# Optimization experiments

Measured on AMD Instinct MI355X. Metric: run time of the kernel, lower is better.

The kernel has to match this reference:

```python
import jax, jax.numpy as jnp
import numpy as np

NQ = 4
NL = 3
# Z-expectation sign table: state axis order = wire order, reshape(-1) => wire 0 is MSB
_bits = (np.arange(2 ** NQ)[:, None] >> np.arange(NQ - 1, -1, -1)) & 1
Z_SIGNS = jnp.asarray((1 - 2 * _bits).astype(np.float32))  # (16, 4)
_CNOT = jnp.asarray(np.array([[1, 0, 0, 0], [0, 1, 0, 0], [0, 0, 0, 1], [0, 0, 1, 0]],
                             dtype=np.complex64).reshape(2, 2, 2, 2))


def _rx(t):
    c = jnp.cos(t / 2).astype(jnp.complex64)
    s = (-1j) * jnp.sin(t / 2).astype(jnp.complex64)
    return jnp.stack([jnp.stack([c, s]), jnp.stack([s, c])])


def _rot(phi, theta, omega):
    # PennyLane Rot = RZ(omega) @ RY(theta) @ RZ(phi)
    ez = jnp.exp(-0.5j * phi.astype(jnp.complex64))
    zero = jnp.zeros_like(ez)
    rz1 = jnp.stack([jnp.stack([ez, zero]), jnp.stack([zero, jnp.conj(ez)])])
    c = jnp.cos(theta / 2).astype(jnp.complex64)
    s = jnp.sin(theta / 2).astype(jnp.complex64)
    ry = jnp.stack([jnp.stack([c, -s]), jnp.stack([s, c])])
    eo = jnp.exp(-0.5j * omega.astype(jnp.complex64))
    rz2 = jnp.stack([jnp.stack([eo, zero]), jnp.stack([zero, jnp.conj(eo)])])
    return rz2 @ ry @ rz1


def _apply1(state, U, wire):
    state = jnp.tensordot(U, state, axes=[[1], [wire]])
    return jnp.moveaxis(state, 0, wire)


def _apply_cnot(state, c, t):
    state = jnp.tensordot(_CNOT, state, axes=[[2, 3], [c, t]])
    return jnp.moveaxis(state, [0, 1], [c, t])


def _circuit(x4, qw):
    state = jnp.zeros((2,) * NQ, jnp.complex64).at[(0,) * NQ].set(1.0)
    for i in range(NQ):
        state = _apply1(state, _rx(x4[i]), i)
    for layer in range(NL):
        for q in range(NQ):
            state = _apply1(state, _rot(qw[layer, q, 0], qw[layer, q, 1], qw[layer, q, 2]), q)
        for q in range(NQ - 1):
            state = _apply_cnot(state, q, q + 1)
    probs = jnp.abs(state.reshape(-1)) ** 2  # (16,)
    return probs @ Z_SIGNS  # (NQ,) PauliZ expectations


def setup_inputs() -> dict:
    key = jax.random.key(0)
    ks = jax.random.split(key, 16)
    D, H1, H2, L = 2048, 128, 64, 32
    B = 16384
    s = 0.02
    return {
        "x": jax.random.normal(ks[0], (B, D), jnp.float32),
        "enc_w0": jax.random.normal(ks[1], (D, H1), jnp.float32) * s,
        "enc_b0": jnp.zeros((H1,), jnp.float32),
        "enc_w1": jax.random.normal(ks[2], (H1, H2), jnp.float32) * s,
        "enc_b1": jnp.zeros((H2,), jnp.float32),
        "enc_w2": jax.random.normal(ks[3], (H2, L), jnp.float32) * s,
        "enc_b2": jnp.zeros((L,), jnp.float32),
        "qw": jax.random.normal(ks[4], (NL, NQ, 3), jnp.float32),
        "dec_w0": jax.random.normal(ks[5], (NQ, H2), jnp.float32) * s,
        "dec_b0": jnp.zeros((H2,), jnp.float32),
        "dec_w1": jax.random.normal(ks[6], (H2, H1), jnp.float32) * s,
        "dec_b1": jnp.zeros((H1,), jnp.float32),
        "dec_w2": jax.random.normal(ks[7], (H1, D), jnp.float32) * s,
        "dec_b2": jnp.zeros((D,), jnp.float32),
    }


def reference(x, enc_w0, enc_b0, enc_w1, enc_b1, enc_w2, enc_b2, qw,
              dec_w0, dec_b0, dec_w1, dec_b1, dec_w2, dec_b2):
    # Encoder (eval mode: dropout is identity)
    h = jax.nn.relu(x @ enc_w0 + enc_b0)
    h = jax.nn.relu(h @ enc_w1 + enc_b1)
    latent = h @ enc_w2 + enc_b2  # (B, 32)
    # Quantum refinement: circuit only reads latent[:, :NQ]
    refined = jax.vmap(lambda xi: _circuit(xi, qw))(latent[:, :NQ]).astype(jnp.float32)  # (B, 4)
    # Decoder
    h = jax.nn.relu(refined @ dec_w0 + dec_b0)
    h = jax.nn.relu(h @ dec_w1 + dec_b1)
    return h @ dec_w2 + dec_b2
```

## Files before the change

### kernel.cpp

```cpp
#include <hip/hip_runtime.h>
#include <hip/hip_bf16.h>

typedef __attribute__((ext_vector_type(8))) short short8;
typedef __attribute__((ext_vector_type(4))) float f32x4;

#define DEVI __device__ __forceinline__

DEVI unsigned short f2bf(float f) {
    union { float f; unsigned u; } v; v.f = f;
    unsigned r = v.u + 0x7FFFu + ((v.u >> 16) & 1u);
    return (unsigned short)(r >> 16);
}

DEVI unsigned cvtpk_bf16(float lo, float hi) {
    float2 t; t.x = lo; t.y = hi;
    __hip_bfloat162 h = __float22bfloat162_rn(t);
    union { __hip_bfloat162 h; unsigned u; } c; c.h = h;
    return c.u;
}

DEVI void gload_lds16(const void* g, void* l) {
    __builtin_amdgcn_global_load_lds(
        (const __attribute__((address_space(1))) unsigned int*)(unsigned long long)g,
        (__attribute__((address_space(3))) unsigned int*)(unsigned int)(unsigned long long)l,
        16, 0, 0);
}

DEVI void run_circuit(const float lat[4], const float* __restrict__ qw, float out4[4])
{
    float cw[4], sw[4];
#pragma unroll
    for (int w = 0; w < 4; ++w) sincosf(0.5f * lat[w], &sw[w], &cw[w]);

    float sr[16], si[16];
#pragma unroll
    for (int s = 0; s < 16; ++s) {
        float mag = 1.f; int p = 0;
#pragma unroll
        for (int w = 0; w < 4; ++w) {
            int b = (s >> (3 - w)) & 1;
            mag *= b ? sw[w] : cw[w];
            p += b;
        }
        p &= 3;
        sr[s] = (p == 0) ? mag : ((p == 2) ? -mag : 0.f);
        si[s] = (p == 1) ? -mag : ((p == 3) ? mag : 0.f);
    }

#pragma unroll
    for (int L = 0; L < 3; ++L) {
#pragma unroll
        for (int q = 0; q < 4; ++q) {
            const float* gq = qw + (L * 4 + q) * 3;
            float phi = gq[0], th = gq[1], om = gq[2];
            float ct, st;
            sincosf(0.5f * th, &st, &ct);
            float ap = 0.5f * (phi + om), am = 0.5f * (phi - om);
            float cap, sap, cam, sam;
            sincosf(ap, &sap, &cap);
            sincosf(am, &sam, &cam);
            float u00r =  ct * cap, u00i = -ct * sap;
            float u01r = -st * cam, u01i = -st * sam;
            float u10r =  st * cam, u10i = -st * sam;
            float u11r =  ct * cap, u11i =  ct * sap;
            int bm = 8 >> q;
#pragma unroll
            for (int i = 0; i < 16; ++i) {
                if (i & bm) continue;
                int j = i | bm;
                float ar = sr[i], ai = si[i], br = sr[j], bi = si[j];
                sr[i] = u00r*ar - u00i*ai + u01r*br - u01i*bi;
                si[i] = u00r*ai + u00i*ar + u01r*bi + u01i*br;
                sr[j] = u10r*ar - u10i*ai + u11r*br - u11i*bi;
                si[j] = u10r*ai + u10i*ar + u11r*bi + u11i*br;
            }
        }
#pragma unroll
        for (int q = 0; q < 3; ++q) {
            int cm = 8 >> q, tm = 8 >> (q + 1);
#pragma unroll
            for (int i = 0; i < 16; ++i) {
                if ((i & cm) && !(i & tm)) {
                    int j = i | tm;
                    float tr = sr[i]; sr[i] = sr[j]; sr[j] = tr;
                    float ti = si[i]; si[i] = si[j]; si[j] = ti;
                }
            }
        }
    }
#pragma unroll
    for (int q = 0; q < 4; ++q) {
        int bm = 8 >> q;
        float e = 0.f;
#pragma unroll
        for (int i = 0; i < 16; ++i) {
            float p = sr[i]*sr[i] + si[i]*si[i];
            e += (i & bm) ? -p : p;
        }
        out4[q] = e;
    }
}

__global__ void prep_kernel(const float* __restrict__ ew0, const float* __restrict__ ew1,
                            const float* __restrict__ dw1, const float* __restrict__ dw2,
                            unsigned short* __restrict__ wsb)
{
    int i = blockIdx.x * 256 + threadIdx.x;
    if (i < 262144) {
        int n = i >> 11, k = i & 2047;
        wsb[i] = f2bf(ew0[k * 128 + n]);
    } else if (i < 270336) {
        int t = i - 262144; int n = t >> 7, k = t & 127;
        wsb[i] = f2bf(ew1[k * 64 + n]);
    } else if (i < 278528) {
        int t = i - 270336; int n = t >> 6, k = t & 63;
        wsb[i] = f2bf(dw1[k * 128 + n]);
    } else if (i < 540672) {
        int t = i - 278528; int n = t >> 7, k = t & 127;
        wsb[i] = f2bf(dw2[k * 2048 + n]);
    }
}

__launch_bounds__(256, 3)
__global__ void fused_kernel(const float* __restrict__ x,
                             const unsigned short* __restrict__ w0T,
                             const float* __restrict__ b0e,
                             const unsigned short* __restrict__ w1eT,
                             const float* __restrict__ b1e,
                             const float* __restrict__ w2e,
                             const float* __restrict__ b2e,
                             const float* __restrict__ qw,
                             const float* __restrict__ w0d,
                             const float* __restrict__ b0d,
                             const unsigned short* __restrict__ w1dT,
                             const float* __restrict__ b1d,
                             const unsigned short* __restrict__ w2T,
                             const float* __restrict__ b2d,
                             float* __restrict__ out)
{
    __shared__ __align__(16) char smem[53376];
    char* const W1E  = smem;
    char* const W1D  = smem + 16384;
    char* const H1   = smem + 32768;
    char* const GA   = smem + 32768;
    float* const H2  = (float*)(smem + 40960);
    char* const HD   = smem + 49280;

    const int tid = threadIdx.x;
    const int lane = tid & 63;
    const int wv = tid >> 6;
    const int wm = wv >> 1, wn = wv & 1;
    const int l16 = lane & 15, lq = lane >> 4;
    const int m0 = blockIdx.x * 32;

    {
        const int rA0 = wv * 8 + (lane >> 4);
        const int rA1 = rA0 + 4;
        const char* sA0 = (const char*)(x + (long)(m0 + rA0) * 2048 + ((lane & 15) ^ (rA0 & 7)) * 4);
        const char* sA1 = (const char*)(x + (long)(m0 + rA1) * 2048 + ((lane & 15) ^ (rA1 & 7)) * 4);
        const int rB0 = wv * 32 +  0 + (lane >> 3);
        const int rB1 = wv * 32 +  8 + (lane >> 3);
        const int rB2 = wv * 32 + 16 + (lane >> 3);
        const int rB3 = wv * 32 + 24 + (lane >> 3);
        const char* sB0 = (const char*)(w0T + rB0 * 2048 + ((lane & 7) ^ (rB0 & 7)) * 8);
        const char* sB1 = (const char*)(w0T + rB1 * 2048 + ((lane & 7) ^ (rB1 & 7)) * 8);
        const char* sB2 = (const char*)(w0T + rB2 * 2048 + ((lane & 7) ^ (rB2 & 7)) * 8);
        const char* sB3 = (const char*)(w0T + rB3 * 2048 + ((lane & 7) ^ (rB3 & 7)) * 8);
        const int aoff0 = wv * 2048;
        const int aoff1 = wv * 2048 + 1024;
        const int boff0 = wv * 4096;
        const int boff1 = wv * 4096 + 1024;
        const int boff2 = wv * 4096 + 2048;
        const int boff3 = wv * 4096 + 3072;

        auto issue = [&](int cur) {
            char* Ab = smem + (cur ? 8192 : 0);
            char* Bb = smem + (cur ? 32768 : 16384);
            gload_lds16(sA0, Ab + aoff0); sA0 += 256;
            gload_lds16(sA1, Ab + aoff1); sA1 += 256;
            gload_lds16(sB0, Bb + boff0); sB0 += 128;
            gload_lds16(sB1, Bb + boff1); sB1 += 128;
            gload_lds16(sB2, Bb + boff2); sB2 += 128;
            gload_lds16(sB3, Bb + boff3); sB3 += 128;
        };

        f32x4 acc[4];
#pragma unroll
        for (int b = 0; b < 4; ++b) acc[b] = (f32x4)(0.f);

        const int arow = wm * 16 + l16;
        const int ah = arow & 7;

        issue(0);
        __syncthreads();

        for (int t = 0; t < 32; ++t) {
            if (t < 31) issue((t + 1) & 1);
            const char* Ab = smem + ((t & 1) ? 8192 : 0);
            const char* Bb = smem + ((t & 1) ? 32768 : 16384);
            const char* abase = Ab + arow * 256;
#pragma unroll
            for (int kk = 0; kk < 2; ++kk) {
                const int c = kk * 8 + lq * 2;
                float4 f0 = *(const float4*)(abase + ((c ^ ah) << 4));
                float4 f1 = *(const float4*)(abase + (((c + 1) ^ ah) << 4));
                union { unsigned u[4]; short8 s; } pk;
                pk.u[0] = cvtpk_bf16(f0.x, f0.y);
                pk.u[1] = cvtpk_bf16(f0.z, f0.w);
                pk.u[2] = cvtpk_bf16(f1.x, f1.y);
                pk.u[3] = cvtpk_bf16(f1.z, f1.w);
                short8 aF = pk.s;
#pragma unroll
                for (int fn = 0; fn < 4; ++fn) {
                    int n = wn * 64 + fn * 16 + l16;
                    short8 bF = *(const short8*)(Bb + n * 128 + (((kk * 4 + lq) ^ (n & 7)) << 4));
                    acc[fn] = __builtin_amdgcn_mfma_f32_16x16x32_bf16(aF, bF, acc[fn], 0, 0, 0);
                }
            }
            __syncthreads();
        }

        {
            const int r16 = wv * 16 + (lane >> 4);
            const int s16 = lane & 15;
            const int r8  = wv * 32 + (lane >> 3);
            const int s8  = lane & 7;
#pragma unroll
            for (int i = 0; i < 4; ++i) {
                int row = r16 + i * 4;
                gload_lds16(w1eT + row * 128 + ((s16 ^ (row & 7)) * 8),
                            W1E + wv * 4096 + i * 1024);
            }
#pragma unroll
            for (int i = 0; i < 4; ++i) {
                int row = r8 + i * 8;
                gload_lds16(w1dT + row * 64 + ((s8 ^ (row & 7)) * 8),
                            W1D + wv * 4096 + i * 1024);
            }
        }

        float b0v[4];
#pragma unroll
        for (int fn = 0; fn < 4; ++fn) b0v[fn] = b0e[wn * 64 + fn * 16 + l16];
#pragma unroll
        for (int fn = 0; fn < 4; ++fn)
#pragma unroll
            for (int r = 0; r < 4; ++r) {
                int row = wm * 16 + lq * 4 + r;
                int col = wn * 64 + fn * 16 + l16;
                float v = fmaxf(acc[fn][r] + b0v[fn], 0.f);
                *(unsigned short*)(H1 + row * 256 + ((((col >> 3) ^ (row & 7)) << 4) | ((col & 7) << 1))) = f2bf(v);
            }
    }
    __syncthreads();

    {
        f32x4 acc2[2];
#pragma unroll
        for (int b = 0; b < 2; ++b) acc2[b] = (f32x4)(0.f);
#pragma unroll
        for (int kk = 0; kk < 4; ++kk) {
            int row = wm * 16 + l16;
            short8 aF = *(const short8*)(H1 + row * 256 + (((kk * 4 + lq) ^ (row & 7)) << 4));
#pragma unroll
            for (int fn = 0; fn < 2; ++fn) {
                int n = wn * 32 + fn * 16 + l16;
                short8 bF = *(const short8*)(W1E + n * 256 + (((kk * 4 + lq) ^ (n & 7)) << 4));
                acc2[fn] = __builtin_amdgcn_mfma_f32_16x16x32_bf16(aF, bF, acc2[fn], 0, 0, 0);
            }
        }
        float b1v[2];
#pragma unroll
        for (int fn = 0; fn < 2; ++fn) b1v[fn] = b1e[wn * 32 + fn * 16 + l16];
#pragma unroll
        for (int fn = 0; fn < 2; ++fn)
#pragma unroll
            for (int r = 0; r < 4; ++r) {
                int row = wm * 16 + lq * 4 + r;
                int col = wn * 32 + fn * 16 + l16;
                H2[row * 65 + col] = fmaxf(acc2[fn][r] + b1v[fn], 0.f);
            }
    }
    __syncthreads();

    if (tid < 32) {
        float lat[4];
#pragma unroll
        for (int j = 0; j < 4; ++j) lat[j] = b2e[j];
        const float* h2row = H2 + tid * 65;
#pragma unroll 8
        for (int k = 0; k < 64; ++k) {
            float hv = h2row[k];
            float4 wv4 = *(const float4*)(w2e + k * 32);
            lat[0] = fmaf(hv, wv4.x, lat[0]);
            lat[1] = fmaf(hv, wv4.y, lat[1]);
            lat[2] = fmaf(hv, wv4.z, lat[2]);
            lat[3] = fmaf(hv, wv4.w, lat[3]);
        }
        float o4[4];
        run_circuit(lat, qw, o4);
#pragma unroll
        for (int s = 0; s < 8; ++s) {
            uint4 pk;
            unsigned tmp[4];
#pragma unroll
            for (int p = 0; p < 4; ++p) {
                int c0 = s * 8 + p * 2;
                float v0 = fmaxf(o4[0]*w0d[c0]     + o4[1]*w0d[64+c0]   + o4[2]*w0d[128+c0]   + o4[3]*w0d[192+c0]   + b0d[c0],   0.f);
                float v1 = fmaxf(o4[0]*w0d[c0+1]   + o4[1]*w0d[64+c0+1] + o4[2]*w0d[128+c0+1] + o4[3]*w0d[192+c0+1] + b0d[c0+1], 0.f);
                tmp[p] = (unsigned)f2bf(v0) | ((unsigned)f2bf(v1) << 16);
            }
            pk.x = tmp[0]; pk.y = tmp[1]; pk.z = tmp[2]; pk.w = tmp[3];
            *(uint4*)(HD + tid * 128 + ((s ^ (tid & 7)) << 4)) = pk;
        }
    }
    __syncthreads();

    {
        f32x4 accg[4];
#pragma unroll
        for (int b = 0; b < 4; ++b) accg[b] = (f32x4)(0.f);
#pragma unroll
        for (int kk = 0; kk < 2; ++kk) {
            int row = wm * 16 + l16;
            short8 aF = *(const short8*)(HD + row * 128 + (((kk * 4 + lq) ^ (row & 7)) << 4));
#pragma unroll
            for (int fn = 0; fn < 4; ++fn) {
                int n = wn * 64 + fn * 16 + l16;
                short8 bF = *(const short8*)(W1D + n * 128 + (((kk * 4 + lq) ^ (n & 7)) << 4));
                accg[fn] = __builtin_amdgcn_mfma_f32_16x16x32_bf16(aF, bF, accg[fn], 0, 0, 0);
            }
        }
        float b1v[4];
#pragma unroll
        for (int fn = 0; fn < 4; ++fn) b1v[fn] = b1d[wn * 64 + fn * 16 + l16];
#pragma unroll
        for (int fn = 0; fn < 4; ++fn)
#pragma unroll
            for (int r = 0; r < 4; ++r) {
                int row = wm * 16 + lq * 4 + r;
                int col = wn * 64 + fn * 16 + l16;
                float v = fmaxf(accg[fn][r] + b1v[fn], 0.f);
                *(unsigned short*)(GA + row * 256 + ((((col >> 3) ^ (row & 7)) << 4) | ((col & 7) << 1))) = f2bf(v);
            }
    }
    __syncthreads();

    {
        auto w2issue = [&](int c) {
            char* W = smem + ((c & 1) ? 16384 : 0);
            int base = c * 64;
#pragma unroll
            for (int i = 0; i < 4; ++i) {
                int row = wv * 16 + i * 4 + (lane >> 4);
                gload_lds16(w2T + (base + row) * 128 + (((lane & 15) ^ (row & 7)) * 8),
                            W + wv * 4096 + i * 1024);
            }
        };
        w2issue(0);
        __syncthreads();

        const int arow = wm * 16 + l16;
        for (int c = 0; c < 32; ++c) {
            if (c < 31) w2issue(c + 1);
            const char* W = smem + ((c & 1) ? 16384 : 0);
            f32x4 a3[2];
#pragma unroll
            for (int b = 0; b < 2; ++b) a3[b] = (f32x4)(0.f);
#pragma unroll
            for (int kk = 0; kk < 4; ++kk) {
                short8 aF = *(const short8*)(GA + arow * 256 + (((kk * 4 + lq) ^ (arow & 7)) << 4));
#pragma unroll
                for (int fn = 0; fn < 2; ++fn) {
                    int n = wn * 32 + fn * 16 + l16;
                    short8 bF = *(const short8*)(W + n * 256 + (((kk * 4 + lq) ^ (n & 7)) << 4));
                    a3[fn] = __builtin_amdgcn_mfma_f32_16x16x32_bf16(aF, bF, a3[fn], 0, 0, 0);
                }
            }
            int n0 = c * 64;
            float b2v[2];
#pragma unroll
            for (int fn = 0; fn < 2; ++fn) b2v[fn] = b2d[n0 + wn * 32 + fn * 16 + l16];
#pragma unroll
            for (int fn = 0; fn < 2; ++fn)
#pragma unroll
                for (int r = 0; r < 4; ++r) {
                    int row = m0 + wm * 16 + lq * 4 + r;
                    int col = n0 + wn * 32 + fn * 16 + l16;
                    __builtin_nontemporal_store(a3[fn][r] + b2v[fn], &out[(long)row * 2048 + col]);
                }
            __syncthreads();
        }
    }
}

extern "C" void kernel_launch(void* const* d_in, const int* in_sizes, int n_in,
                              void* d_out, int out_size, void* d_ws, size_t ws_size,
                              hipStream_t stream)
{
    (void)in_sizes; (void)n_in; (void)out_size; (void)ws_size;
    const float* x      = (const float*)d_in[0];
    const float* enc_w0 = (const float*)d_in[1];
    const float* enc_b0 = (const float*)d_in[2];
    const float* enc_w1 = (const float*)d_in[3];
    const float* enc_b1 = (const float*)d_in[4];
    const float* enc_w2 = (const float*)d_in[5];
    const float* enc_b2 = (const float*)d_in[6];
    const float* qw     = (const float*)d_in[7];
    const float* dec_w0 = (const float*)d_in[8];
    const float* dec_b0 = (const float*)d_in[9];
    const float* dec_w1 = (const float*)d_in[10];
    const float* dec_b1 = (const float*)d_in[11];
    const float* dec_w2 = (const float*)d_in[12];
    const float* dec_b2 = (const float*)d_in[13];

    unsigned short* wsb = (unsigned short*)d_ws;

    prep_kernel<<<2112, 256, 0, stream>>>(enc_w0, enc_w1, dec_w1, dec_w2, wsb);
    fused_kernel<<<512, 256, 0, stream>>>(x, wsb, enc_b0,
                                          wsb + 262144, enc_b1, enc_w2, enc_b2, qw,
                                          dec_w0, dec_b0, wsb + 270336, dec_b1,
                                          wsb + 278528, dec_b2, (float*)d_out);
}
```

Baseline: 105.1 us.

## Halve rows per block to 16 and launch 1024 blocks with smaller LDS

Each block now handles 16 batch rows instead of 32, and the four waves split the N dimension instead of a 2x2 M/N grid. The grid doubles to 1024 blocks, LDS shrinks from about 53KB to 40KB with regions reused across stages, and launch bounds rise to 4 blocks per CU. The aim is more parallelism and occupancy across the 256 CUs. The cost is that every block re-streams the full 2048x128 enc_w0 and dec_w2 weights for half as many rows, doubling weight traffic through L2. The output stores also drop the nontemporal hint.

```diff
diff --git a/kernel.cpp b/kernel.cpp
--- a/kernel.cpp
+++ b/kernel.cpp
@@ -121,7 +121,7 @@
     }
 }
 
-__launch_bounds__(256, 3)
+__launch_bounds__(256, 4)
 __global__ void fused_kernel(const float* __restrict__ x,
                              const unsigned short* __restrict__ w0T,
                              const float* __restrict__ b0e,
@@ -138,26 +138,23 @@
                              const float* __restrict__ b2d,
                              float* __restrict__ out)
 {
-    __shared__ __align__(16) char smem[53376];
-    char* const W1E  = smem;
-    char* const W1D  = smem + 16384;
-    char* const H1   = smem + 32768;
-    char* const GA   = smem + 32768;
-    float* const H2  = (float*)(smem + 40960);
-    char* const HD   = smem + 49280;
+    __shared__ __align__(16) char smem[40960];
+    char* const W1E = smem;
+    char* const W1D = smem + 16384;
+    char* const H1  = smem + 32768;
+    float* const H2 = (float*)(smem + 36864);
+    char* const HD  = smem;
+    char* const GA  = smem + 2048;
 
     const int tid = threadIdx.x;
     const int lane = tid & 63;
     const int wv = tid >> 6;
-    const int wm = wv >> 1, wn = wv & 1;
     const int l16 = lane & 15, lq = lane >> 4;
-    const int m0 = blockIdx.x * 32;
+    const int m0 = blockIdx.x * 16;
 
     {
-        const int rA0 = wv * 8 + (lane >> 4);
-        const int rA1 = rA0 + 4;
-        const char* sA0 = (const char*)(x + (long)(m0 + rA0) * 2048 + ((lane & 15) ^ (rA0 & 7)) * 4);
-        const char* sA1 = (const char*)(x + (long)(m0 + rA1) * 2048 + ((lane & 15) ^ (rA1 & 7)) * 4);
+        const int rA = wv * 4 + (lane >> 4);
+        const char* sA = (const char*)(x + (long)(m0 + rA) * 2048 + ((lane & 15) ^ (rA & 7)) * 4);
         const int rB0 = wv * 32 +  0 + (lane >> 3);
         const int rB1 = wv * 32 +  8 + (lane >> 3);
         const int rB2 = wv * 32 + 16 + (lane >> 3);
@@ -166,29 +163,27 @@
         const char* sB1 = (const char*)(w0T + rB1 * 2048 + ((lane & 7) ^ (rB1 & 7)) * 8);
         const char* sB2 = (const char*)(w0T + rB2 * 2048 + ((lane & 7) ^ (rB2 & 7)) * 8);
         const char* sB3 = (const char*)(w0T + rB3 * 2048 + ((lane & 7) ^ (rB3 & 7)) * 8);
-        const int aoff0 = wv * 2048;
-        const int aoff1 = wv * 2048 + 1024;
+        const int aoff  = wv * 1024;
         const int boff0 = wv * 4096;
         const int boff1 = wv * 4096 + 1024;
         const int boff2 = wv * 4096 + 2048;
         const int boff3 = wv * 4096 + 3072;
 
         auto issue = [&](int cur) {
-            char* Ab = smem + (cur ? 8192 : 0);
-            char* Bb = smem + (cur ? 32768 : 16384);
-            gload_lds16(sA0, Ab + aoff0); sA0 += 256;
-            gload_lds16(sA1, Ab + aoff1); sA1 += 256;
+            char* Ab = smem + (cur ? 4096 : 0);
+            char* Bb = smem + (cur ? 24576 : 8192);
+            gload_lds16(sA, Ab + aoff);   sA  += 256;
             gload_lds16(sB0, Bb + boff0); sB0 += 128;
             gload_lds16(sB1, Bb + boff1); sB1 += 128;
             gload_lds16(sB2, Bb + boff2); sB2 += 128;
             gload_lds16(sB3, Bb + boff3); sB3 += 128;
         };
 
-        f32x4 acc[4];
-#pragma unroll
-        for (int b = 0; b < 4; ++b) acc[b] = (f32x4)(0.f);
-
-        const int arow = wm * 16 + l16;
+        f32x4 acc[2];
+#pragma unroll
+        for (int b = 0; b < 2; ++b) acc[b] = (f32x4)(0.f);
+
+        const int arow = l16;
         const int ah = arow & 7;
 
         issue(0);
@@ -196,8 +191,8 @@
 
         for (int t = 0; t < 32; ++t) {
             if (t < 31) issue((t + 1) & 1);
-            const char* Ab = smem + ((t & 1) ? 8192 : 0);
-            const char* Bb = smem + ((t & 1) ? 32768 : 16384);
+            const char* Ab = smem + ((t & 1) ? 4096 : 0);
+            const char* Bb = smem + ((t & 1) ? 24576 : 8192);
             const char* abase = Ab + arow * 256;
 #pragma unroll
             for (int kk = 0; kk < 2; ++kk) {
@@ -211,8 +206,8 @@
                 pk.u[3] = cvtpk_bf16(f1.z, f1.w);
                 short8 aF = pk.s;
 #pragma unroll
-                for (int fn = 0; fn < 4; ++fn) {
-                    int n = wn * 64 + fn * 16 + l16;
+                for (int fn = 0; fn < 2; ++fn) {
+                    int n = wv * 32 + fn * 16 + l16;
                     short8 bF = *(const short8*)(Bb + n * 128 + (((kk * 4 + lq) ^ (n & 7)) << 4));
                     acc[fn] = __builtin_amdgcn_mfma_f32_16x16x32_bf16(aF, bF, acc[fn], 0, 0, 0);
                 }
@@ -239,15 +234,15 @@
             }
         }
 
-        float b0v[4];
-#pragma unroll
-        for (int fn = 0; fn < 4; ++fn) b0v[fn] = b0e[wn * 64 + fn * 16 + l16];
-#pragma unroll
-        for (int fn = 0; fn < 4; ++fn)
+        float b0v[2];
+#pragma unroll
+        for (int fn = 0; fn < 2; ++fn) b0v[fn] = b0e[wv * 32 + fn * 16 + l16];
+#pragma unroll
+        for (int fn = 0; fn < 2; ++fn)
 #pragma unroll
             for (int r = 0; r < 4; ++r) {
-                int row = wm * 16 + lq * 4 + r;
-                int col = wn * 64 + fn * 16 + l16;
+                int row = lq * 4 + r;
+                int col = wv * 32 + fn * 16 + l16;
                 float v = fmaxf(acc[fn][r] + b0v[fn], 0.f);
                 *(unsigned short*)(H1 + row * 256 + ((((col >> 3) ^ (row & 7)) << 4) | ((col & 7) << 1))) = f2bf(v);
             }
@@ -255,39 +250,30 @@
     __syncthreads();
 
     {
-        f32x4 acc2[2];
-#pragma unroll
-        for (int b = 0; b < 2; ++b) acc2[b] = (f32x4)(0.f);
+        f32x4 acc2 = (f32x4)(0.f);
 #pragma unroll
         for (int kk = 0; kk < 4; ++kk) {
-            int row = wm * 16 + l16;
+            int row = l16;
             short8 aF = *(const short8*)(H1 + row * 256 + (((kk * 4 + lq) ^ (row & 7)) << 4));
-#pragma unroll
-            for (int fn = 0; fn < 2; ++fn) {
-                int n = wn * 32 + fn * 16 + l16;
-                short8 bF = *(const short8*)(W1E + n * 256 + (((kk * 4 + lq) ^ (n & 7)) << 4));
-                acc2[fn] = __builtin_amdgcn_mfma_f32_16x16x32_bf16(aF, bF, acc2[fn], 0, 0, 0);
-            }
-        }
-        float b1v[2];
-#pragma unroll
-        for (int fn = 0; fn < 2; ++fn) b1v[fn] = b1e[wn * 32 + fn * 16 + l16];
-#pragma unroll
-        for (int fn = 0; fn < 2; ++fn)
-#pragma unroll
-            for (int r = 0; r < 4; ++r) {
-                int row = wm * 16 + lq * 4 + r;
-                int col = wn * 32 + fn * 16 + l16;
-                H2[row * 65 + col] = fmaxf(acc2[fn][r] + b1v[fn], 0.f);
-            }
+            int n = wv * 16 + l16;
+            short8 bF = *(const short8*)(W1E + n * 256 + (((kk * 4 + lq) ^ (n & 7)) << 4));
+            acc2 = __builtin_amdgcn_mfma_f32_16x16x32_bf16(aF, bF, acc2, 0, 0, 0);
+        }
+        float b1v = b1e[wv * 16 + l16];
+#pragma unroll
+        for (int r = 0; r < 4; ++r) {
+            int row = lq * 4 + r;
+            int col = wv * 16 + l16;
+            H2[row * 64 + col] = fmaxf(acc2[r] + b1v, 0.f);
+        }
     }
     __syncthreads();
 
-    if (tid < 32) {
+    if (tid < 16) {
         float lat[4];
 #pragma unroll
         for (int j = 0; j < 4; ++j) lat[j] = b2e[j];
-        const float* h2row = H2 + tid * 65;
+        const float* h2row = H2 + tid * 64;
 #pragma unroll 8
         for (int k = 0; k < 64; ++k) {
             float hv = h2row[k];
@@ -317,29 +303,29 @@
     __syncthreads();
 
     {
-        f32x4 accg[4];
-#pragma unroll
-        for (int b = 0; b < 4; ++b) accg[b] = (f32x4)(0.f);
+        f32x4 accg[2];
+#pragma unroll
+        for (int b = 0; b < 2; ++b) accg[b] = (f32x4)(0.f);
 #pragma unroll
         for (int kk = 0; kk < 2; ++kk) {
-            int row = wm * 16 + l16;
+            int row = l16;
             short8 aF = *(const short8*)(HD + row * 128 + (((kk * 4 + lq) ^ (row & 7)) << 4));
 #pragma unroll
-            for (int fn = 0; fn < 4; ++fn) {
-                int n = wn * 64 + fn * 16 + l16;
+            for (int fn = 0; fn < 2; ++fn) {
+                int n = wv * 32 + fn * 16 + l16;
                 short8 bF = *(const short8*)(W1D + n * 128 + (((kk * 4 + lq) ^ (n & 7)) << 4));
                 accg[fn] = __builtin_amdgcn_mfma_f32_16x16x32_bf16(aF, bF, accg[fn], 0, 0, 0);
             }
         }
-        float b1v[4];
-#pragma unroll
-        for (int fn = 0; fn < 4; ++fn) b1v[fn] = b1d[wn * 64 + fn * 16 + l16];
-#pragma unroll
-        for (int fn = 0; fn < 4; ++fn)
+        float b1v[2];
+#pragma unroll
+        for (int fn = 0; fn < 2; ++fn) b1v[fn] = b1d[wv * 32 + fn * 16 + l16];
+#pragma unroll
+        for (int fn = 0; fn < 2; ++fn)
 #pragma unroll
             for (int r = 0; r < 4; ++r) {
-                int row = wm * 16 + lq * 4 + r;
-                int col = wn * 64 + fn * 16 + l16;
+                int row = lq * 4 + r;
+                int col = wv * 32 + fn * 16 + l16;
                 float v = fmaxf(accg[fn][r] + b1v[fn], 0.f);
                 *(unsigned short*)(GA + row * 256 + ((((col >> 3) ^ (row & 7)) << 4) | ((col & 7) << 1))) = f2bf(v);
             }
@@ -348,7 +334,7 @@
 
     {
         auto w2issue = [&](int c) {
-            char* W = smem + ((c & 1) ? 16384 : 0);
+            char* W = smem + ((c & 1) ? 24576 : 8192);
             int base = c * 64;
 #pragma unroll
             for (int i = 0; i < 4; ++i) {
@@ -360,35 +346,26 @@
         w2issue(0);
         __syncthreads();
 
-        const int arow = wm * 16 + l16;
+        const int arow = l16;
         for (int c = 0; c < 32; ++c) {
             if (c < 31) w2issue(c + 1);
-            const char* W = smem + ((c & 1) ? 16384 : 0);
-            f32x4 a3[2];
-#pragma unroll
-            for (int b = 0; b < 2; ++b) a3[b] = (f32x4)(0.f);
+            const char* W = smem + ((c & 1) ? 24576 : 8192);
+            f32x4 a3 = (f32x4)(0.f);
 #pragma unroll
             for (int kk = 0; kk < 4; ++kk) {
                 short8 aF = *(const short8*)(GA + arow * 256 + (((kk * 4 + lq) ^ (arow & 7)) << 4));
-#pragma unroll
-                for (int fn = 0; fn < 2; ++fn) {
-                    int n = wn * 32 + fn * 16 + l16;
-                    short8 bF = *(const short8*)(W + n * 256 + (((kk * 4 + lq) ^ (n & 7)) << 4));
-                    a3[fn] = __builtin_amdgcn_mfma_f32_16x16x32_bf16(aF, bF, a3[fn], 0, 0, 0);
-                }
+                int n = wv * 16 + l16;
+                short8 bF = *(const short8*)(W + n * 256 + (((kk * 4 + lq) ^ (n & 7)) << 4));
+                a3 = __builtin_amdgcn_mfma_f32_16x16x32_bf16(aF, bF, a3, 0, 0, 0);
             }
             int n0 = c * 64;
-            float b2v[2];
-#pragma unroll
-            for (int fn = 0; fn < 2; ++fn) b2v[fn] = b2d[n0 + wn * 32 + fn * 16 + l16];
-#pragma unroll
-            for (int fn = 0; fn < 2; ++fn)
-#pragma unroll
-                for (int r = 0; r < 4; ++r) {
-                    int row = m0 + wm * 16 + lq * 4 + r;
-                    int col = n0 + wn * 32 + fn * 16 + l16;
-                    __builtin_nontemporal_store(a3[fn][r] + b2v[fn], &out[(long)row * 2048 + col]);
-                }
+            float b2v = b2d[n0 + wv * 16 + l16];
+#pragma unroll
+            for (int r = 0; r < 4; ++r) {
+                int row = m0 + lq * 4 + r;
+                int col = n0 + wv * 16 + l16;
+                out[(long)row * 2048 + col] = a3[r] + b2v;
+            }
             __syncthreads();
         }
     }
@@ -417,8 +394,8 @@
     unsigned short* wsb = (unsigned short*)d_ws;
 
     prep_kernel<<<2112, 256, 0, stream>>>(enc_w0, enc_w1, dec_w1, dec_w2, wsb);
-    fused_kernel<<<512, 256, 0, stream>>>(x, wsb, enc_b0,
-                                          wsb + 262144, enc_b1, enc_w2, enc_b2, qw,
-                                          dec_w0, dec_b0, wsb + 270336, dec_b1,
-                                          wsb + 278528, dec_b2, (float*)d_out);
-}
+    fused_kernel<<<1024, 256, 0, stream>>>(x, wsb, enc_b0,
+                                           wsb + 262144, enc_b1, enc_w2, enc_b2, qw,
+                                           dec_w0, dec_b0, wsb + 270336, dec_b1,
+                                           wsb + 278528, dec_b2, (float*)d_out);
+}
```

New measurement: 148.7 us. +41.4%, slower.
